# Performance work log

Measured on AMD Instinct MI355X. Metric: run time of the kernel, lower is better.

Reference implementation:

```python
import jax, jax.numpy as jnp
import numpy as np

N, L, S, E, A, D = 16, 256, 128, 128, 9, 768
ARG_ROLES = 23      # score width = ARG_ROLES + 1
MAX_ARG = 9         # hard-coded max_len_arg in the torch module
N_HID = 768


def setup_inputs() -> dict:
    key = jax.random.key(0)
    ks = jax.random.split(key, 10)
    all_embeddings = jax.random.normal(ks[0], (N, L, D), jnp.float32)
    # last-3-layer BERT attention maps, 12 heads, positive entries
    attn_last3 = jax.random.uniform(ks[1], (3, N, 12, L, L), jnp.float32)
    # per-sample sorted distinct first-subword indices (all positive, full length:
    # the ragged filter idxs>0 then keeps everything -> fixed-shape gather)
    idx_keys = jax.random.split(ks[2], N)
    cand = jnp.arange(1, L - MAX_ARG - 1)
    idxs_to_collect = jax.vmap(
        lambda k: jnp.sort(jax.random.choice(k, cand, (S + 2,), replace=False))
    )(idx_keys).astype(jnp.int32)
    is_triggers = (jax.random.uniform(ks[3], (N, S)) < 0.05).astype(jnp.float32)
    is_triggers = is_triggers.at[:, 0].set(1.0)  # >=1 trigger per sample
    entity_mapping = jax.random.normal(ks[4], (N, S, E), jnp.float32) * 0.05
    arg_weight_matrices = jax.random.normal(ks[5], (N, MAX_ARG, A), jnp.float32) * 0.3
    map_keys = jax.random.split(ks[6], N)
    arg_mapping = jax.vmap(
        lambda k: jax.random.permutation(k, ARG_ROLES + 1)[:A]
    )(map_keys).astype(jnp.int32)
    W1 = jax.random.normal(ks[7], (6 * D, N_HID), jnp.float32) * 0.02
    b1 = jnp.zeros((N_HID,), jnp.float32)
    W2 = jax.random.normal(ks[8], (N_HID, 1), jnp.float32) * 0.02
    b2 = jnp.zeros((1,), jnp.float32)
    return {
        "all_embeddings": all_embeddings,
        "attn_last3": attn_last3,
        "entity_mapping": entity_mapping,
        "arg_weight_matrices": arg_weight_matrices,
        "is_triggers": is_triggers,
        "W1": W1, "b1": b1, "W2": W2, "b2": b2,
        "idxs_to_collect": idxs_to_collect,
        "arg_mapping": arg_mapping,
    }


def reference(all_embeddings, attn_last3, entity_mapping, arg_weight_matrices,
              is_triggers, W1, b1, W2, b2, idxs_to_collect, arg_mapping):
    sqrt_d = jnp.sqrt(jnp.asarray(D, jnp.float32))
    sent_idx = idxs_to_collect[:, :S]                      # [N,S] first-subword ids
    # get_fist_subword_embeddings: ragged gather (full-length here)
    sent_emb = jnp.take_along_axis(all_embeddings, sent_idx[:, :, None], axis=1)  # [N,S,D]
    # arg-type tokens sit right after the second-to-last [SEP]
    arg_pos = idxs_to_collect[:, -2:-1] + 1 + jnp.arange(MAX_ARG)[None, :]        # [N,9]
    arg_raw = jnp.take_along_axis(all_embeddings, arg_pos[:, :, None], axis=1)    # [N,9,D]

    entity_emb = jnp.einsum('nsd,nse->ned', sent_emb, entity_mapping)             # [N,E,D]
    trig = jnp.sum(sent_emb * is_triggers[..., None], axis=1) \
           / jnp.sum(is_triggers, axis=1, keepdims=True)                          # [N,D]
    del trig  # _trigger is computed but unused downstream in the torch forward
    arg_emb = jnp.einsum('nkd,nka->nad', arg_raw, arg_weight_matrices)            # [N,A,D]

    # bi-attention scores (broadcast-mul-sum == contraction over D)
    t2a = jnp.einsum('ned,nad->nea', entity_emb, arg_emb) / sqrt_d
    w = (t2a - 5.0) / 2.0                                                         # [N,E,A]
    token_argAwared = jnp.einsum('nea,nad->ned', w, arg_emb)                      # [N,E,D]
    arg_tokenAwared = jnp.einsum('nea,ned->nad', w, entity_emb)                   # [N,A,D]

    # select_hidden_att for each of the last 3 layers
    att_mean = jnp.mean(attn_last3, axis=2)                                       # [3,N,L,L]
    def sel_layer(a):  # a: [N,L,L] -> row/col gather + row renorm
        s = jax.vmap(lambda m, i: m[i][:, i])(a, sent_idx)                        # [N,S,S]
        return s / (jnp.sum(s, axis=-1, keepdims=True) + 1e-9)
    t2t = (sel_layer(att_mean[0]) + sel_layer(att_mean[1]) + sel_layer(att_mean[2])) / 3.0

    h2h_sent = jnp.einsum('nst,ntd->nsd', t2t, sent_emb)                          # [N,S,D]
    # A_h2h and H_ are projected from sent space (S) to entity space (E)
    A_h2h_e = jnp.einsum('nsd,nse->ned', h2h_sent, entity_mapping)                # [N,E,D]
    H_e = entity_emb                                                              # sent_emb projected == entity_emb

    a2a = jax.nn.softmax(jnp.einsum('nad,nbd->nab', arg_emb, arg_emb), axis=-1)   # [N,A,A]
    u2u = jnp.einsum('nab,nbd->nad', a2a, arg_emb)                                # [N,A,D]

    shp = (N, E, A, D)
    H_    = jnp.broadcast_to(H_e[:, :, None, :], shp)
    U_    = jnp.broadcast_to(arg_emb[:, None, :, :], shp)
    A_h2u = jnp.broadcast_to(token_argAwared[:, :, None, :], shp)
    A_h2h = jnp.broadcast_to(A_h2h_e[:, :, None, :], shp)
    A_u2h = jnp.broadcast_to(arg_tokenAwared[:, None, :, :], shp)
    A_u2u = jnp.broadcast_to(u2u[:, None, :, :], shp)
    latent = jnp.concatenate([H_, U_, A_h2u, A_h2h, A_u2h, A_u2u], axis=-1)       # [N,E,A,6D]

    hid = jax.nn.gelu(latent @ W1 + b1, approximate=False)                        # [N,E,A,768]
    score = (hid @ W2 + b2)[..., 0]                                               # [N,E,A]

    # map_arg_to_ids: scatter each arg slot back to its global role id
    def scatter_one(s, ids):  # s [E,A], ids [A]
        return jnp.full((E, ARG_ROLES + 1), -1e6, jnp.float32).at[:, ids].set(s)
    new_score = jax.vmap(scatter_one)(score, arg_mapping)                         # [N,E,24]
    return new_score
```

## Files before the change

### kernel.cpp

```cpp
#include <hip/hip_runtime.h>
#include <math.h>

namespace {
constexpr int N_ = 16, L_ = 256, S_ = 128, E_ = 128, A_ = 9, D_ = 768, H_ = 768, RO_ = 24;
constexpr int IDXW = 130;
constexpr int W1R = 6 * D_;
constexpr float INV_SQRT_D = 0.03608439182435161f;
constexpr int PESZ = 2048 * 768;
constexpr int PASZ = 144 * 768;
constexpr int GB_T2T    = 0;
constexpr int GB_W1T    = 1024;
constexpr int GB_GATHER = 1888;
constexpr int GB_ENTMAP = 2080;
constexpr int GB_ARGU   = 2096;
constexpr int GB_TOTAL  = 2112;
}

using bshort8 = __attribute__((ext_vector_type(8))) short;
using f32x4v = __attribute__((ext_vector_type(4))) float;

__device__ __forceinline__ unsigned short f2bf(float f) {
    unsigned u = __builtin_bit_cast(unsigned, f);
    return (unsigned short)((u + 0x7fffu + ((u >> 16) & 1u)) >> 16);
}

__device__ __forceinline__ void gemm_body128(const unsigned short* __restrict__ A,
                                             const unsigned short* __restrict__ BT,
                                             int lda, int ldb, int c0, int tid,
                                             short (*As)[40], short (*Bs)[40],
                                             f32x4v acc[2][4]) {
    const int wave = tid >> 6, lane = tid & 63;
    const int row16 = lane & 15, quad = lane >> 4;
    for (int k0 = 0; k0 < S_; k0 += 32) {
#pragma unroll
        for (int i = 0; i < 2; ++i) {
            const int idx = tid + 256 * i;
            const int r = idx >> 2, q = idx & 3;
            *reinterpret_cast<bshort8*>(&As[r][q * 8]) =
                *reinterpret_cast<const bshort8*>(A + (size_t)r * lda + k0 + q * 8);
        }
        {
            const int col = tid >> 2, q = tid & 3;
            *reinterpret_cast<bshort8*>(&Bs[col][q * 8]) =
                *reinterpret_cast<const bshort8*>(BT + (size_t)(c0 + col) * ldb + k0 + q * 8);
        }
        __syncthreads();
        bshort8 a[2], b[4];
#pragma unroll
        for (int mi = 0; mi < 2; ++mi)
            a[mi] = *reinterpret_cast<const bshort8*>(&As[wave * 32 + mi * 16 + row16][quad * 8]);
#pragma unroll
        for (int ni = 0; ni < 4; ++ni)
            b[ni] = *reinterpret_cast<const bshort8*>(&Bs[ni * 16 + row16][quad * 8]);
#pragma unroll
        for (int mi = 0; mi < 2; ++mi)
#pragma unroll
            for (int ni = 0; ni < 4; ++ni)
                acc[mi][ni] = __builtin_amdgcn_mfma_f32_16x16x32_bf16(a[mi], b[ni], acc[mi][ni], 0, 0, 0);
        __syncthreads();
    }
}

__global__ __launch_bounds__(256) void stage1_k(const float* __restrict__ all_emb,
                                                const int* __restrict__ idxs,
                                                const float* __restrict__ ent_map,
                                                const float* __restrict__ W1,
                                                const float* __restrict__ argw,
                                                const float* __restrict__ attn,
                                                unsigned short* __restrict__ sentT,
                                                unsigned short* __restrict__ entmapT,
                                                short* __restrict__ W1t,
                                                unsigned short* __restrict__ t2tT,
                                                float* __restrict__ argE,
                                                unsigned short* __restrict__ argEbf,
                                                unsigned short* __restrict__ u2ubf) {
    __shared__ __align__(16) unsigned char smem[33792];
    const int b = blockIdx.x, tid = threadIdx.x;

    if (b < GB_W1T) {
        const int idx = b - GB_T2T;
        const int n = idx >> 6;
        const int half = tid >> 7, t128 = tid & 127;
        const int s0 = (idx & 63) << 1;
        const int s = s0 | half;
        const int w = t128 >> 6, lane = tid & 63;
        float* sum2 = (float*)smem;
        float* part = (float*)(smem + 12288);
        unsigned short* tileT = (unsigned short*)(smem + 12544);
        const int is = idxs[n * IDXW + s], it = idxs[n * IDXW + t128];
#pragma unroll
        for (int l = 0; l < 3; ++l) {
            const float* base = attn + ((size_t)((l * N_ + n) * 12 + w * 6)) * (L_ * L_)
                              + (size_t)is * L_ + lane * 4;
            float4 acc = {0.f, 0.f, 0.f, 0.f};
#pragma unroll
            for (int h = 0; h < 6; ++h) {
                const float4 v = *reinterpret_cast<const float4*>(base + (size_t)h * (L_ * L_));
                acc.x += v.x; acc.y += v.y; acc.z += v.z; acc.w += v.w;
            }
            *reinterpret_cast<float4*>(&sum2[(((half * 3 + l) * 2 + w) << 8) + lane * 4]) = acc;
        }
        __syncthreads();
        float m[3];
#pragma unroll
        for (int l = 0; l < 3; ++l) {
            m[l] = (sum2[(((half * 3 + l) * 2 + 0) << 8) + it] +
                    sum2[(((half * 3 + l) * 2 + 1) << 8) + it]) * (1.0f / 12.0f);
            float r = m[l];
#pragma unroll
            for (int off = 32; off; off >>= 1) r += __shfl_xor(r, off, 64);
            if (lane == 0) part[(half * 3 + l) * 2 + w] = r;
        }
        __syncthreads();
        float out = 0.f;
#pragma unroll
        for (int l = 0; l < 3; ++l)
            out += m[l] / (part[(half * 3 + l) * 2 + 0] + part[(half * 3 + l) * 2 + 1] + 1e-9f);
        tileT[t128 * 2 + half] = f2bf(out * (1.0f / 3.0f));
        __syncthreads();
        if (tid < 128) {
            const unsigned int v = ((const unsigned int*)tileT)[tid];
            *reinterpret_cast<unsigned int*>(t2tT + ((size_t)(n * S_) + tid) * S_ + s0) = v;
        }
    } else if (b < GB_GATHER) {
        const int b2 = b - GB_W1T;
        const int k0 = (b2 % 72) * 64, h0 = (b2 / 72) * 64;
        auto tile = (float (*)[65])smem;
        const int tx = tid & 63, ty = tid >> 6;
#pragma unroll
        for (int i = 0; i < 16; ++i) {
            const int r = ty + i * 4;
            tile[r][tx] = W1[(size_t)(k0 + r) * H_ + h0 + tx];
        }
        __syncthreads();
#pragma unroll
        for (int i = 0; i < 16; ++i) {
            const int r = ty + i * 4;
            W1t[(size_t)(h0 + r) * W1R + k0 + tx] = (short)f2bf(tile[tx][r]);
        }
    } else if (b < GB_ENTMAP) {
        const int b2 = b - GB_GATHER;
        const int n = b2 / 12, d0 = (b2 % 12) * 64;
        auto tile = (unsigned short (*)[132])smem;
#pragma unroll
        for (int it = 0; it < 8; ++it) {
            const int lin = tid + 256 * it;
            const int s = lin >> 4, dq = (lin & 15) * 4;
            const int row = idxs[n * IDXW + s];
            const float4 v = *reinterpret_cast<const float4*>(all_emb + ((size_t)(n * L_ + row)) * D_ + d0 + dq);
            tile[dq + 0][s] = f2bf(v.x); tile[dq + 1][s] = f2bf(v.y);
            tile[dq + 2][s] = f2bf(v.z); tile[dq + 3][s] = f2bf(v.w);
        }
        __syncthreads();
#pragma unroll
        for (int it = 0; it < 8; ++it) {
            const int lin = tid + 256 * it;
            const int d = lin >> 5, s4 = (lin & 31) * 4;
            ushort4 v = {tile[d][s4], tile[d][s4 + 1], tile[d][s4 + 2], tile[d][s4 + 3]};
            *reinterpret_cast<ushort4*>(sentT + ((size_t)(n * D_) + d0 + d) * S_ + s4) = v;
        }
    } else if (b < GB_ARGU) {
        const int n = b - GB_ENTMAP;
        auto tile = (unsigned short (*)[132])smem;
#pragma unroll
        for (int it = 0; it < 16; ++it) {
            const int lin = tid + 256 * it;
            const int s = lin >> 5, eq = (lin & 31) * 4;
            const float4 v = *reinterpret_cast<const float4*>(ent_map + ((size_t)(n * S_ + s)) * E_ + eq);
            tile[eq + 0][s] = f2bf(v.x); tile[eq + 1][s] = f2bf(v.y);
            tile[eq + 2][s] = f2bf(v.z); tile[eq + 3][s] = f2bf(v.w);
        }
        __syncthreads();
#pragma unroll
        for (int it = 0; it < 16; ++it) {
            const int lin = tid + 256 * it;
            const int e = lin >> 5, s4 = (lin & 31) * 4;
            ushort4 v = {tile[e][s4], tile[e][s4 + 1], tile[e][s4 + 2], tile[e][s4 + 3]};
            *reinterpret_cast<ushort4*>(entmapT + ((size_t)(n * E_) + e) * S_ + s4) = v;
        }
    } else {
        const int n = b - GB_ARGU;
        auto wsm = (float (*)[A_])smem;
        auto part45 = (float (*)[4])(smem + 512);
        auto Psm = (float (*)[A_])(smem + 1536);
        if (tid < A_ * A_) wsm[tid / A_][tid % A_] = argw[n * A_ * A_ + tid];
        __syncthreads();
        const int p0 = idxs[n * IDXW + S_] + 1;
        float pp[45] = {};
        float vals[3][A_];
#pragma unroll
        for (int c = 0; c < 3; ++c) {
            const int d = tid + 256 * c;
            float raw[A_];
#pragma unroll
            for (int k = 0; k < A_; ++k) raw[k] = all_emb[((size_t)(n * L_ + p0 + k)) * D_ + d];
#pragma unroll
            for (int a = 0; a < A_; ++a) {
                float acc = 0.f;
#pragma unroll
                for (int k = 0; k < A_; ++k) acc = fmaf(raw[k], wsm[k][a], acc);
                vals[c][a] = acc;
                argE[((size_t)(n * A_ + a)) * D_ + d] = acc;
                argEbf[((size_t)(n * A_ + a)) * D_ + d] = f2bf(acc);
            }
            int p = 0;
#pragma unroll
            for (int a = 0; a < A_; ++a)
#pragma unroll
                for (int bb = a; bb < A_; ++bb) pp[p++] += vals[c][a] * vals[c][bb];
        }
        const int lane = tid & 63, wv = tid >> 6;
#pragma unroll
        for (int p = 0; p < 45; ++p) {
            float v = pp[p];
            for (int off = 32; off; off >>= 1) v += __shfl_down(v, off, 64);
            if (lane == 0) part45[p][wv] = v;
        }
        __syncthreads();
        if (tid < 45) part45[tid][0] = part45[tid][0] + part45[tid][1] + part45[tid][2] + part45[tid][3];
        __syncthreads();
        if (tid < A_) {
            const int a = tid;
            float v[A_], mx = -1e30f;
#pragma unroll
            for (int bb = 0; bb < A_; ++bb) {
                const int lo = a < bb ? a : bb, hi = a < bb ? bb : a;
                v[bb] = part45[lo * (19 - lo) / 2 + hi - lo][0];
                mx = fmaxf(mx, v[bb]);
            }
            float sm = 0.f;
#pragma unroll
            for (int bb = 0; bb < A_; ++bb) { v[bb] = expf(v[bb] - mx); sm += v[bb]; }
            const float inv = 1.0f / sm;
#pragma unroll
            for (int bb = 0; bb < A_; ++bb) Psm[a][bb] = v[bb] * inv;
        }
        __syncthreads();
#pragma unroll
        for (int c = 0; c < 3; ++c) {
            const int d = tid + 256 * c;
#pragma unroll
            for (int a = 0; a < A_; ++a) {
                float acc = 0.f;
#pragma unroll
                for (int bb = 0; bb < A_; ++bb) acc = fmaf(Psm[a][bb], vals[c][bb], acc);
                u2ubf[((size_t)(n * A_ + a)) * D_ + d] = f2bf(acc);
            }
        }
    }
}

__global__ __launch_bounds__(256) void gemm_entM1_k(const unsigned short* __restrict__ entmapT,
                                                    const unsigned short* __restrict__ sentT,
                                                    const unsigned short* __restrict__ t2tT,
                                                    float* __restrict__ entf,
                                                    unsigned short* __restrict__ entbf,
                                                    unsigned short* __restrict__ M1bf) {
    __shared__ __align__(16) short As[128][40];
    __shared__ __align__(16) short Bs[64][40];
    const int bx = blockIdx.x, tid = threadIdx.x;
    const int wave = tid >> 6, lane = tid & 63;
    const int row16 = lane & 15, quad = lane >> 4;
    f32x4v acc[2][4] = {};
    if (bx < 192) {
        const int n = bx / 12, c0 = (bx % 12) * 64;
        gemm_body128(entmapT + (size_t)n * S_ * S_, sentT + (size_t)n * D_ * S_,
                     S_, S_, c0, tid, As, Bs, acc);
#pragma unroll
        for (int mi = 0; mi < 2; ++mi)
#pragma unroll
            for (int ni = 0; ni < 4; ++ni) {
                const int rbase = wave * 32 + mi * 16 + quad * 4;
                const int col = c0 + ni * 16 + row16;
#pragma unroll
                for (int t = 0; t < 4; ++t) {
                    const size_t o = ((size_t)(n * S_) + rbase + t) * D_ + col;
                    entf[o] = acc[mi][ni][t];
                    entbf[o] = f2bf(acc[mi][ni][t]);
                }
            }
    } else {
        const int idx = bx - 192;
        const int n = idx >> 1, c0 = (idx & 1) * 64;
        gemm_body128(entmapT + (size_t)n * S_ * S_, t2tT + (size_t)n * S_ * S_,
                     S_, S_, c0, tid, As, Bs, acc);
#pragma unroll
        for (int mi = 0; mi < 2; ++mi)
#pragma unroll
            for (int ni = 0; ni < 4; ++ni) {
                const int rbase = wave * 32 + mi * 16 + quad * 4;
                const int col = c0 + ni * 16 + row16;
#pragma unroll
                for (int t = 0; t < 4; ++t)
                    M1bf[((size_t)(n * S_) + rbase + t) * S_ + col] = f2bf(acc[mi][ni][t]);
            }
    }
}

__global__ __launch_bounds__(256) void fused3_k(const unsigned short* __restrict__ M1bf,
                                                const unsigned short* __restrict__ sentT,
                                                const float* __restrict__ entf,
                                                const float* __restrict__ argE,
                                                unsigned short* __restrict__ Ah2hbf,
                                                unsigned short* __restrict__ tokAbf,
                                                unsigned short* __restrict__ argTbf) {
    __shared__ __align__(16) unsigned char smem[15872];
    const int bx = blockIdx.x, tid = threadIdx.x;
    if (bx < N_ * A_) {
        const int n = bx / A_, a = bx % A_;
        float* argS = (float*)smem;
        float* wl = (float*)(smem + 3072);
        for (int i = tid; i < D_; i += 256) argS[i] = argE[((size_t)(n * A_ + a)) * D_ + i];
        __syncthreads();
        {
            const int e = tid >> 1, h = tid & 1;
            const float* er = entf + ((size_t)(n * E_ + e)) * D_ + h * 384;
            float p = 0.f;
            for (int d = 0; d < 384; ++d) p = fmaf(er[d], argS[h * 384 + d], p);
            p += __shfl_down(p, 1, 64);
            if (h == 0) wl[e] = (p * INV_SQRT_D - 5.0f) * 0.5f;
        }
        __syncthreads();
        const float* eb = entf + (size_t)n * E_ * D_;
#pragma unroll
        for (int c = 0; c < 3; ++c) {
            const int d = tid + 256 * c;
            float acc = 0.f;
            for (int e = 0; e < E_; ++e) acc = fmaf(wl[e], eb[(size_t)e * D_ + d], acc);
            argTbf[((size_t)(n * A_ + a)) * D_ + d] = f2bf(acc);
        }
    } else if (bx < N_ * A_ + 192) {
        const int idx = bx - N_ * A_;
        const int n = idx / 12, c0 = (idx % 12) * 64;
        short (*As)[40] = (short (*)[40])smem;
        short (*Bs)[40] = (short (*)[40])(smem + 10240);
        const int wave = tid >> 6, lane = tid & 63;
        const int row16 = lane & 15, quad = lane >> 4;
        f32x4v acc[2][4] = {};
        gemm_body128(M1bf + (size_t)n * S_ * S_, sentT + (size_t)n * D_ * S_,
                     S_, S_, c0, tid, As, Bs, acc);
#pragma unroll
        for (int mi = 0; mi < 2; ++mi)
#pragma unroll
            for (int ni = 0; ni < 4; ++ni) {
                const int rbase = wave * 32 + mi * 16 + quad * 4;
                const int col = c0 + ni * 16 + row16;
#pragma unroll
                for (int t = 0; t < 4; ++t)
                    Ah2hbf[((size_t)(n * S_) + rbase + t) * D_ + col] = f2bf(acc[mi][ni][t]);
            }
    } else {
        const int idx = bx - (N_ * A_ + 192);
        const int n = idx >> 7, e = idx & 127;
        float* wl = (float*)smem;
        float* part = (float*)(smem + 64);
        const float* er = entf + ((size_t)(n * E_ + e)) * D_;
        const float* ar = argE + (size_t)n * A_ * D_;
        float acc[A_] = {};
        for (int d = tid; d < D_; d += 256) {
            const float ev = er[d];
#pragma unroll
            for (int a = 0; a < A_; ++a) acc[a] = fmaf(ev, ar[(size_t)a * D_ + d], acc[a]);
        }
        const int lane = tid & 63, wv = tid >> 6;
#pragma unroll
        for (int a = 0; a < A_; ++a)
            for (int off = 32; off; off >>= 1) acc[a] += __shfl_down(acc[a], off, 64);
        if (lane == 0)
            for (int a = 0; a < A_; ++a) part[a * 4 + wv] = acc[a];
        __syncthreads();
        if (tid < A_)
            wl[tid] = ((part[tid * 4] + part[tid * 4 + 1] + part[tid * 4 + 2] + part[tid * 4 + 3])
                       * INV_SQRT_D - 5.0f) * 0.5f;
        __syncthreads();
#pragma unroll
        for (int c = 0; c < 3; ++c) {
            const int d = tid + 256 * c;
            float s = 0.f;
#pragma unroll
            for (int a = 0; a < A_; ++a) s = fmaf(wl[a], ar[(size_t)a * D_ + d], s);
            tokAbf[((size_t)(n * E_ + e)) * D_ + d] = f2bf(s);
        }
    }
}

__global__ __launch_bounds__(256) void mfma_mlp_k(const unsigned short* __restrict__ e0,
                                                  const unsigned short* __restrict__ e1,
                                                  const unsigned short* __restrict__ e2,
                                                  const unsigned short* __restrict__ a0,
                                                  const unsigned short* __restrict__ a1,
                                                  const unsigned short* __restrict__ a2,
                                                  const short* __restrict__ W1t,
                                                  float* __restrict__ Pe3, float* __restrict__ Pa3) {
    __shared__ __align__(16) short As[128][40];
    __shared__ __align__(16) short Bs[64][40];
    const int c0 = blockIdx.x * 64;
    const int by = blockIdx.y;
    const int seg = by / 18;
    const int blk = by % 18;
    const bool isPa = blk >= 16;
    const unsigned short* Aseg;
    int woff;
    if (isPa) {
        Aseg = seg == 0 ? a0 : (seg == 1 ? a1 : a2);
        woff = seg == 0 ? 1 * D_ : (seg == 1 ? 4 * D_ : 5 * D_);
    } else {
        Aseg = seg == 0 ? e0 : (seg == 1 ? e1 : e2);
        woff = seg == 0 ? 0 : (seg == 1 ? 2 * D_ : 3 * D_);
    }
    const int M = isPa ? N_ * A_ : N_ * E_;
    const int r0 = (isPa ? blk - 16 : blk) * 128;
    float* C = isPa ? (Pa3 + (size_t)seg * PASZ) : (Pe3 + (size_t)seg * PESZ);
    const int tid = threadIdx.x;
    const int wave = tid >> 6, lane = tid & 63;
    const int row16 = lane & 15, quad = lane >> 4;
    f32x4v acc[2][4] = {};
    for (int kk = 0; kk < D_; kk += 32) {
#pragma unroll
        for (int i = 0; i < 2; ++i) {
            const int idx = tid + 256 * i;
            const int r = idx >> 2, q = idx & 3;
            bshort8 av = {};
            if (r0 + r < M) av = *reinterpret_cast<const bshort8*>(Aseg + (size_t)(r0 + r) * D_ + kk + q * 8);
            *reinterpret_cast<bshort8*>(&As[r][q * 8]) = av;
        }
        {
            const int col = tid >> 2, q = tid & 3;
            *reinterpret_cast<bshort8*>(&Bs[col][q * 8]) =
                *reinterpret_cast<const bshort8*>(W1t + (size_t)(c0 + col) * W1R + woff + kk + q * 8);
        }
        __syncthreads();
        bshort8 a[2], b[4];
#pragma unroll
        for (int mi = 0; mi < 2; ++mi)
            a[mi] = *reinterpret_cast<const bshort8*>(&As[wave * 32 + mi * 16 + row16][quad * 8]);
#pragma unroll
        for (int ni = 0; ni < 4; ++ni)
            b[ni] = *reinterpret_cast<const bshort8*>(&Bs[ni * 16 + row16][quad * 8]);
#pragma unroll
        for (int mi = 0; mi < 2; ++mi)
#pragma unroll
            for (int ni = 0; ni < 4; ++ni)
                acc[mi][ni] = __builtin_amdgcn_mfma_f32_16x16x32_bf16(a[mi], b[ni], acc[mi][ni], 0, 0, 0);
        __syncthreads();
    }
#pragma unroll
    for (int mi = 0; mi < 2; ++mi) {
#pragma unroll
        for (int ni = 0; ni < 4; ++ni) {
            const int rbase = r0 + wave * 32 + mi * 16 + quad * 4;
            const int col = c0 + ni * 16 + row16;
#pragma unroll
            for (int t = 0; t < 4; ++t)
                if (rbase + t < M) C[(size_t)(rbase + t) * H_ + col] = acc[mi][ni][t];
        }
    }
}

__global__ __launch_bounds__(256) void score_k(const float* __restrict__ Pe3, const float* __restrict__ Pa3,
                                               const float* __restrict__ b1, const float* __restrict__ W2,
                                               const float* __restrict__ b2, const int* __restrict__ arg_map,
                                               float* __restrict__ out) {
    const int n = blockIdx.x >> 7, e = blockIdx.x & 127;
    const int tid = threadIdx.x;
    __shared__ float paS[A_ * H_];
    __shared__ float part[A_][4];
    float* orow = out + ((size_t)(n * E_ + e)) * RO_;
    if (tid < RO_) orow[tid] = -1000000.0f;
    for (int i = tid; i < A_ * H_; i += 256) {
        const size_t o = (size_t)n * A_ * H_ + i;
        paS[i] = Pa3[o] + Pa3[PASZ + o] + Pa3[2 * PASZ + o];
    }
    __syncthreads();
    const size_t ro = ((size_t)(n * E_ + e)) * H_;
    float acc[A_] = {};
    for (int h = tid; h < H_; h += 256) {
        const float pe = Pe3[ro + h] + Pe3[PESZ + ro + h] + Pe3[2 * PESZ + ro + h] + b1[h];
        const float w2 = W2[h];
#pragma unroll
        for (int a = 0; a < A_; ++a) {
            const float x = pe + paS[a * H_ + h];
            const float g = x * 0.5f * (1.0f + erff(x * 0.70710678118654752f));
            acc[a] = fmaf(g, w2, acc[a]);
        }
    }
    const int lane = tid & 63, wv = tid >> 6;
#pragma unroll
    for (int a = 0; a < A_; ++a)
        for (int off = 32; off; off >>= 1) acc[a] += __shfl_down(acc[a], off, 64);
    if (lane == 0)
        for (int a = 0; a < A_; ++a) part[a][wv] = acc[a];
    __syncthreads();
    if (tid < A_) {
        const float s = part[tid][0] + part[tid][1] + part[tid][2] + part[tid][3] + b2[0];
        orow[arg_map[n * A_ + tid]] = s;
    }
}

extern "C" void kernel_launch(void* const* d_in, const int* in_sizes, int n_in,
                              void* d_out, int out_size, void* d_ws, size_t ws_size,
                              hipStream_t stream) {
    const float* all_emb = (const float*)d_in[0];
    const float* attn    = (const float*)d_in[1];
    const float* ent_map = (const float*)d_in[2];
    const float* argw    = (const float*)d_in[3];
    const float* W1 = (const float*)d_in[5];
    const float* b1 = (const float*)d_in[6];
    const float* W2 = (const float*)d_in[7];
    const float* b2 = (const float*)d_in[8];
    const int* idxs    = (const int*)d_in[9];
    const int* arg_map = (const int*)d_in[10];
    float* out = (float*)d_out;

    float* ws = (float*)d_ws;
    float* entf = ws + 0;
    float* Pe3  = ws + 1572864;
    float* argE = ws + 6291456;
    float* Pa3  = ws + 6402048;
    short*          W1t     = (short*)(ws + 6733824);
    unsigned short* sentT   = (unsigned short*)(ws + 8503296);
    unsigned short* entmapT = (unsigned short*)(ws + 9289728);
    unsigned short* t2tT    = (unsigned short*)(ws + 9420800);
    unsigned short* M1bf    = (unsigned short*)(ws + 9551872);
    unsigned short* argEbf  = (unsigned short*)(ws + 9682944);
    unsigned short* u2ubf   = (unsigned short*)(ws + 9738240);
    unsigned short* entbf   = (unsigned short*)(ws + 9793536);
    unsigned short* Ah2hbf  = (unsigned short*)(ws + 10579968);
    unsigned short* tokAbf  = (unsigned short*)(ws + 11366400);
    unsigned short* argTbf  = (unsigned short*)(ws + 12152832);

    stage1_k<<<GB_TOTAL, 256, 0, stream>>>(all_emb, idxs, ent_map, W1, argw, attn,
                                           sentT, entmapT, W1t, t2tT, argE, argEbf, u2ubf);

    gemm_entM1_k<<<224, 256, 0, stream>>>(entmapT, sentT, t2tT, entf, entbf, M1bf);

    fused3_k<<<N_ * A_ + 192 + N_ * E_, 256, 0, stream>>>(M1bf, sentT, entf, argE,
                                                          Ah2hbf, tokAbf, argTbf);

    mfma_mlp_k<<<dim3(12, 54), 256, 0, stream>>>(entbf, tokAbf, Ah2hbf, argEbf, argTbf, u2ubf, W1t, Pe3, Pa3);

    score_k<<<N_ * E_, 256, 0, stream>>>(Pe3, Pa3, b1, W2, b2, arg_map, out);

    (void)in_sizes; (void)n_in; (void)out_size; (void)ws_size;
}
```

Before: 329.7 us.

## Fuse five stage kernels into one persistent kernel with grid barriers

```diff
diff --git a/kernel.cpp b/kernel.cpp
--- a/kernel.cpp
+++ b/kernel.cpp
@@ -24,6 +24,26 @@
     return (unsigned short)((u + 0x7fffu + ((u >> 16) & 1u)) >> 16);
 }
 
+__device__ __forceinline__ void gbar(unsigned* bar) {
+    __syncthreads();
+    if (threadIdx.x == 0) {
+        __threadfence();
+        const unsigned g = __hip_atomic_load(&bar[1], __ATOMIC_RELAXED, __HIP_MEMORY_SCOPE_AGENT);
+        const unsigned a = __hip_atomic_fetch_add(&bar[0], 1u, __ATOMIC_ACQ_REL, __HIP_MEMORY_SCOPE_AGENT);
+        if (a == gridDim.x - 1) {
+            __hip_atomic_store(&bar[0], 0u, __ATOMIC_RELAXED, __HIP_MEMORY_SCOPE_AGENT);
+            __hip_atomic_fetch_add(&bar[1], 1u, __ATOMIC_RELEASE, __HIP_MEMORY_SCOPE_AGENT);
+        } else {
+            unsigned spins = 0;
+            while (__hip_atomic_load(&bar[1], __ATOMIC_ACQUIRE, __HIP_MEMORY_SCOPE_AGENT) == g) {
+                if (++spins > 0x40000000u) break;
+            }
+        }
+        __threadfence();
+    }
+    __syncthreads();
+}
+
 __device__ __forceinline__ void gemm_body128(const unsigned short* __restrict__ A,
                                              const unsigned short* __restrict__ BT,
                                              int lda, int ldb, int c0, int tid,
@@ -61,306 +81,417 @@
     }
 }
 
-__global__ __launch_bounds__(256) void stage1_k(const float* __restrict__ all_emb,
-                                                const int* __restrict__ idxs,
-                                                const float* __restrict__ ent_map,
-                                                const float* __restrict__ W1,
-                                                const float* __restrict__ argw,
-                                                const float* __restrict__ attn,
-                                                unsigned short* __restrict__ sentT,
-                                                unsigned short* __restrict__ entmapT,
-                                                short* __restrict__ W1t,
-                                                unsigned short* __restrict__ t2tT,
-                                                float* __restrict__ argE,
-                                                unsigned short* __restrict__ argEbf,
-                                                unsigned short* __restrict__ u2ubf) {
+__global__ __launch_bounds__(256) void mega_k(
+    const float* __restrict__ all_emb, const float* __restrict__ attn,
+    const float* __restrict__ ent_map, const float* __restrict__ argw,
+    const float* __restrict__ W1, const float* __restrict__ b1,
+    const float* __restrict__ W2, const float* __restrict__ b2,
+    const int* __restrict__ idxs, const int* __restrict__ arg_map,
+    float* __restrict__ out,
+    float* __restrict__ entf, float* __restrict__ Pe3, float* __restrict__ argE,
+    float* __restrict__ Pa3, float* __restrict__ wbuf,
+    short* __restrict__ W1t,
+    unsigned short* __restrict__ sentT, unsigned short* __restrict__ entmapT,
+    unsigned short* __restrict__ t2tT, unsigned short* __restrict__ M1bf,
+    unsigned short* __restrict__ argEbf, unsigned short* __restrict__ u2ubf,
+    unsigned short* __restrict__ entbf, unsigned short* __restrict__ Ah2hbf,
+    unsigned short* __restrict__ tokAbf, unsigned short* __restrict__ argTbf,
+    unsigned* bar) {
     __shared__ __align__(16) unsigned char smem[33792];
-    const int b = blockIdx.x, tid = threadIdx.x;
-
-    if (b < GB_W1T) {
-        const int idx = b - GB_T2T;
-        const int n = idx >> 6;
-        const int half = tid >> 7, t128 = tid & 127;
-        const int s0 = (idx & 63) << 1;
-        const int s = s0 | half;
-        const int w = t128 >> 6, lane = tid & 63;
-        float* sum2 = (float*)smem;
-        float* part = (float*)(smem + 12288);
-        unsigned short* tileT = (unsigned short*)(smem + 12544);
-        const int is = idxs[n * IDXW + s], it = idxs[n * IDXW + t128];
-#pragma unroll
-        for (int l = 0; l < 3; ++l) {
-            const float* base = attn + ((size_t)((l * N_ + n) * 12 + w * 6)) * (L_ * L_)
-                              + (size_t)is * L_ + lane * 4;
-            float4 acc = {0.f, 0.f, 0.f, 0.f};
-#pragma unroll
-            for (int h = 0; h < 6; ++h) {
-                const float4 v = *reinterpret_cast<const float4*>(base + (size_t)h * (L_ * L_));
-                acc.x += v.x; acc.y += v.y; acc.z += v.z; acc.w += v.w;
-            }
-            *reinterpret_cast<float4*>(&sum2[(((half * 3 + l) * 2 + w) << 8) + lane * 4]) = acc;
-        }
-        __syncthreads();
-        float m[3];
-#pragma unroll
-        for (int l = 0; l < 3; ++l) {
-            m[l] = (sum2[(((half * 3 + l) * 2 + 0) << 8) + it] +
-                    sum2[(((half * 3 + l) * 2 + 1) << 8) + it]) * (1.0f / 12.0f);
-            float r = m[l];
-#pragma unroll
-            for (int off = 32; off; off >>= 1) r += __shfl_xor(r, off, 64);
-            if (lane == 0) part[(half * 3 + l) * 2 + w] = r;
-        }
-        __syncthreads();
-        float out = 0.f;
-#pragma unroll
-        for (int l = 0; l < 3; ++l)
-            out += m[l] / (part[(half * 3 + l) * 2 + 0] + part[(half * 3 + l) * 2 + 1] + 1e-9f);
-        tileT[t128 * 2 + half] = f2bf(out * (1.0f / 3.0f));
-        __syncthreads();
-        if (tid < 128) {
-            const unsigned int v = ((const unsigned int*)tileT)[tid];
-            *reinterpret_cast<unsigned int*>(t2tT + ((size_t)(n * S_) + tid) * S_ + s0) = v;
-        }
-    } else if (b < GB_GATHER) {
-        const int b2 = b - GB_W1T;
-        const int k0 = (b2 % 72) * 64, h0 = (b2 / 72) * 64;
-        auto tile = (float (*)[65])smem;
-        const int tx = tid & 63, ty = tid >> 6;
-#pragma unroll
-        for (int i = 0; i < 16; ++i) {
-            const int r = ty + i * 4;
-            tile[r][tx] = W1[(size_t)(k0 + r) * H_ + h0 + tx];
-        }
-        __syncthreads();
-#pragma unroll
-        for (int i = 0; i < 16; ++i) {
-            const int r = ty + i * 4;
-            W1t[(size_t)(h0 + r) * W1R + k0 + tx] = (short)f2bf(tile[tx][r]);
-        }
-    } else if (b < GB_ENTMAP) {
-        const int b2 = b - GB_GATHER;
-        const int n = b2 / 12, d0 = (b2 % 12) * 64;
-        auto tile = (unsigned short (*)[132])smem;
-#pragma unroll
-        for (int it = 0; it < 8; ++it) {
-            const int lin = tid + 256 * it;
-            const int s = lin >> 4, dq = (lin & 15) * 4;
-            const int row = idxs[n * IDXW + s];
-            const float4 v = *reinterpret_cast<const float4*>(all_emb + ((size_t)(n * L_ + row)) * D_ + d0 + dq);
-            tile[dq + 0][s] = f2bf(v.x); tile[dq + 1][s] = f2bf(v.y);
-            tile[dq + 2][s] = f2bf(v.z); tile[dq + 3][s] = f2bf(v.w);
-        }
-        __syncthreads();
-#pragma unroll
-        for (int it = 0; it < 8; ++it) {
-            const int lin = tid + 256 * it;
-            const int d = lin >> 5, s4 = (lin & 31) * 4;
-            ushort4 v = {tile[d][s4], tile[d][s4 + 1], tile[d][s4 + 2], tile[d][s4 + 3]};
-            *reinterpret_cast<ushort4*>(sentT + ((size_t)(n * D_) + d0 + d) * S_ + s4) = v;
-        }
-    } else if (b < GB_ARGU) {
-        const int n = b - GB_ENTMAP;
-        auto tile = (unsigned short (*)[132])smem;
-#pragma unroll
-        for (int it = 0; it < 16; ++it) {
-            const int lin = tid + 256 * it;
-            const int s = lin >> 5, eq = (lin & 31) * 4;
-            const float4 v = *reinterpret_cast<const float4*>(ent_map + ((size_t)(n * S_ + s)) * E_ + eq);
-            tile[eq + 0][s] = f2bf(v.x); tile[eq + 1][s] = f2bf(v.y);
-            tile[eq + 2][s] = f2bf(v.z); tile[eq + 3][s] = f2bf(v.w);
-        }
-        __syncthreads();
-#pragma unroll
-        for (int it = 0; it < 16; ++it) {
-            const int lin = tid + 256 * it;
-            const int e = lin >> 5, s4 = (lin & 31) * 4;
-            ushort4 v = {tile[e][s4], tile[e][s4 + 1], tile[e][s4 + 2], tile[e][s4 + 3]};
-            *reinterpret_cast<ushort4*>(entmapT + ((size_t)(n * E_) + e) * S_ + s4) = v;
-        }
-    } else {
-        const int n = b - GB_ARGU;
-        auto wsm = (float (*)[A_])smem;
-        auto part45 = (float (*)[4])(smem + 512);
-        auto Psm = (float (*)[A_])(smem + 1536);
-        if (tid < A_ * A_) wsm[tid / A_][tid % A_] = argw[n * A_ * A_ + tid];
-        __syncthreads();
-        const int p0 = idxs[n * IDXW + S_] + 1;
-        float pp[45] = {};
-        float vals[3][A_];
-#pragma unroll
-        for (int c = 0; c < 3; ++c) {
-            const int d = tid + 256 * c;
-            float raw[A_];
-#pragma unroll
-            for (int k = 0; k < A_; ++k) raw[k] = all_emb[((size_t)(n * L_ + p0 + k)) * D_ + d];
-#pragma unroll
-            for (int a = 0; a < A_; ++a) {
-                float acc = 0.f;
-#pragma unroll
-                for (int k = 0; k < A_; ++k) acc = fmaf(raw[k], wsm[k][a], acc);
-                vals[c][a] = acc;
-                argE[((size_t)(n * A_ + a)) * D_ + d] = acc;
-                argEbf[((size_t)(n * A_ + a)) * D_ + d] = f2bf(acc);
-            }
-            int p = 0;
-#pragma unroll
-            for (int a = 0; a < A_; ++a)
-#pragma unroll
-                for (int bb = a; bb < A_; ++bb) pp[p++] += vals[c][a] * vals[c][bb];
-        }
-        const int lane = tid & 63, wv = tid >> 6;
-#pragma unroll
-        for (int p = 0; p < 45; ++p) {
-            float v = pp[p];
-            for (int off = 32; off; off >>= 1) v += __shfl_down(v, off, 64);
-            if (lane == 0) part45[p][wv] = v;
-        }
-        __syncthreads();
-        if (tid < 45) part45[tid][0] = part45[tid][0] + part45[tid][1] + part45[tid][2] + part45[tid][3];
-        __syncthreads();
-        if (tid < A_) {
-            const int a = tid;
-            float v[A_], mx = -1e30f;
-#pragma unroll
-            for (int bb = 0; bb < A_; ++bb) {
-                const int lo = a < bb ? a : bb, hi = a < bb ? bb : a;
-                v[bb] = part45[lo * (19 - lo) / 2 + hi - lo][0];
-                mx = fmaxf(mx, v[bb]);
-            }
-            float sm = 0.f;
-#pragma unroll
-            for (int bb = 0; bb < A_; ++bb) { v[bb] = expf(v[bb] - mx); sm += v[bb]; }
-            const float inv = 1.0f / sm;
-#pragma unroll
-            for (int bb = 0; bb < A_; ++bb) Psm[a][bb] = v[bb] * inv;
-        }
-        __syncthreads();
-#pragma unroll
-        for (int c = 0; c < 3; ++c) {
-            const int d = tid + 256 * c;
-#pragma unroll
-            for (int a = 0; a < A_; ++a) {
-                float acc = 0.f;
-#pragma unroll
-                for (int bb = 0; bb < A_; ++bb) acc = fmaf(Psm[a][bb], vals[c][bb], acc);
-                u2ubf[((size_t)(n * A_ + a)) * D_ + d] = f2bf(acc);
-            }
-        }
-    }
-}
-
-__global__ __launch_bounds__(256) void gemm_entM1_k(const unsigned short* __restrict__ entmapT,
-                                                    const unsigned short* __restrict__ sentT,
-                                                    const unsigned short* __restrict__ t2tT,
-                                                    float* __restrict__ entf,
-                                                    unsigned short* __restrict__ entbf,
-                                                    unsigned short* __restrict__ M1bf) {
-    __shared__ __align__(16) short As[128][40];
-    __shared__ __align__(16) short Bs[64][40];
-    const int bx = blockIdx.x, tid = threadIdx.x;
-    const int wave = tid >> 6, lane = tid & 63;
-    const int row16 = lane & 15, quad = lane >> 4;
-    f32x4v acc[2][4] = {};
-    if (bx < 192) {
-        const int n = bx / 12, c0 = (bx % 12) * 64;
-        gemm_body128(entmapT + (size_t)n * S_ * S_, sentT + (size_t)n * D_ * S_,
-                     S_, S_, c0, tid, As, Bs, acc);
-#pragma unroll
-        for (int mi = 0; mi < 2; ++mi)
-#pragma unroll
-            for (int ni = 0; ni < 4; ++ni) {
-                const int rbase = wave * 32 + mi * 16 + quad * 4;
-                const int col = c0 + ni * 16 + row16;
-#pragma unroll
-                for (int t = 0; t < 4; ++t) {
-                    const size_t o = ((size_t)(n * S_) + rbase + t) * D_ + col;
-                    entf[o] = acc[mi][ni][t];
-                    entbf[o] = f2bf(acc[mi][ni][t]);
-                }
-            }
-    } else {
-        const int idx = bx - 192;
-        const int n = idx >> 1, c0 = (idx & 1) * 64;
-        gemm_body128(entmapT + (size_t)n * S_ * S_, t2tT + (size_t)n * S_ * S_,
-                     S_, S_, c0, tid, As, Bs, acc);
-#pragma unroll
-        for (int mi = 0; mi < 2; ++mi)
-#pragma unroll
-            for (int ni = 0; ni < 4; ++ni) {
-                const int rbase = wave * 32 + mi * 16 + quad * 4;
-                const int col = c0 + ni * 16 + row16;
-#pragma unroll
-                for (int t = 0; t < 4; ++t)
-                    M1bf[((size_t)(n * S_) + rbase + t) * S_ + col] = f2bf(acc[mi][ni][t]);
-            }
-    }
-}
-
-__global__ __launch_bounds__(256) void fused3_k(const unsigned short* __restrict__ M1bf,
-                                                const unsigned short* __restrict__ sentT,
-                                                const float* __restrict__ entf,
-                                                const float* __restrict__ argE,
-                                                unsigned short* __restrict__ Ah2hbf,
-                                                unsigned short* __restrict__ tokAbf,
-                                                unsigned short* __restrict__ argTbf) {
-    __shared__ __align__(16) unsigned char smem[15872];
-    const int bx = blockIdx.x, tid = threadIdx.x;
-    if (bx < N_ * A_) {
-        const int n = bx / A_, a = bx % A_;
-        float* argS = (float*)smem;
-        float* wl = (float*)(smem + 3072);
-        for (int i = tid; i < D_; i += 256) argS[i] = argE[((size_t)(n * A_ + a)) * D_ + i];
-        __syncthreads();
-        {
-            const int e = tid >> 1, h = tid & 1;
-            const float* er = entf + ((size_t)(n * E_ + e)) * D_ + h * 384;
-            float p = 0.f;
-            for (int d = 0; d < 384; ++d) p = fmaf(er[d], argS[h * 384 + d], p);
-            p += __shfl_down(p, 1, 64);
-            if (h == 0) wl[e] = (p * INV_SQRT_D - 5.0f) * 0.5f;
-        }
-        __syncthreads();
-        const float* eb = entf + (size_t)n * E_ * D_;
-#pragma unroll
-        for (int c = 0; c < 3; ++c) {
-            const int d = tid + 256 * c;
-            float acc = 0.f;
-            for (int e = 0; e < E_; ++e) acc = fmaf(wl[e], eb[(size_t)e * D_ + d], acc);
-            argTbf[((size_t)(n * A_ + a)) * D_ + d] = f2bf(acc);
-        }
-    } else if (bx < N_ * A_ + 192) {
-        const int idx = bx - N_ * A_;
-        const int n = idx / 12, c0 = (idx % 12) * 64;
+    const int G = gridDim.x, tid = threadIdx.x;
+
+    for (int b = blockIdx.x; b < GB_TOTAL; b += G) {
+        if (b < GB_W1T) {
+            const int idx = b - GB_T2T;
+            const int n = idx >> 6;
+            const int half = tid >> 7, t128 = tid & 127;
+            const int s0 = (idx & 63) << 1;
+            const int s = s0 | half;
+            const int w = t128 >> 6, lane = tid & 63;
+            float* sum2 = (float*)smem;
+            float* part = (float*)(smem + 12288);
+            unsigned short* tileT = (unsigned short*)(smem + 12544);
+            const int is = idxs[n * IDXW + s], it = idxs[n * IDXW + t128];
+#pragma unroll
+            for (int l = 0; l < 3; ++l) {
+                const float* base = attn + ((size_t)((l * N_ + n) * 12 + w * 6)) * (L_ * L_)
+                                  + (size_t)is * L_ + lane * 4;
+                float4 acc = {0.f, 0.f, 0.f, 0.f};
+#pragma unroll
+                for (int h = 0; h < 6; ++h) {
+                    const float4 v = *reinterpret_cast<const float4*>(base + (size_t)h * (L_ * L_));
+                    acc.x += v.x; acc.y += v.y; acc.z += v.z; acc.w += v.w;
+                }
+                *reinterpret_cast<float4*>(&sum2[(((half * 3 + l) * 2 + w) << 8) + lane * 4]) = acc;
+            }
+            __syncthreads();
+            float m[3];
+#pragma unroll
+            for (int l = 0; l < 3; ++l) {
+                m[l] = (sum2[(((half * 3 + l) * 2 + 0) << 8) + it] +
+                        sum2[(((half * 3 + l) * 2 + 1) << 8) + it]) * (1.0f / 12.0f);
+                float r = m[l];
+#pragma unroll
+                for (int off = 32; off; off >>= 1) r += __shfl_xor(r, off, 64);
+                if (lane == 0) part[(half * 3 + l) * 2 + w] = r;
+            }
+            __syncthreads();
+            float o = 0.f;
+#pragma unroll
+            for (int l = 0; l < 3; ++l)
+                o += m[l] / (part[(half * 3 + l) * 2 + 0] + part[(half * 3 + l) * 2 + 1] + 1e-9f);
+            tileT[t128 * 2 + half] = f2bf(o * (1.0f / 3.0f));
+            __syncthreads();
+            if (tid < 128) {
+                const unsigned int v = ((const unsigned int*)tileT)[tid];
+                *reinterpret_cast<unsigned int*>(t2tT + ((size_t)(n * S_) + tid) * S_ + s0) = v;
+            }
+        } else if (b < GB_GATHER) {
+            const int b2 = b - GB_W1T;
+            const int k0 = (b2 % 72) * 64, h0 = (b2 / 72) * 64;
+            auto tile = (float (*)[65])smem;
+            const int tx = tid & 63, ty = tid >> 6;
+#pragma unroll
+            for (int i = 0; i < 16; ++i) {
+                const int r = ty + i * 4;
+                tile[r][tx] = W1[(size_t)(k0 + r) * H_ + h0 + tx];
+            }
+            __syncthreads();
+#pragma unroll
+            for (int i = 0; i < 16; ++i) {
+                const int r = ty + i * 4;
+                W1t[(size_t)(h0 + r) * W1R + k0 + tx] = (short)f2bf(tile[tx][r]);
+            }
+        } else if (b < GB_ENTMAP) {
+            const int b2 = b - GB_GATHER;
+            const int n = b2 / 12, d0 = (b2 % 12) * 64;
+            auto tile = (unsigned short (*)[132])smem;
+#pragma unroll
+            for (int it = 0; it < 8; ++it) {
+                const int lin = tid + 256 * it;
+                const int s = lin >> 4, dq = (lin & 15) * 4;
+                const int row = idxs[n * IDXW + s];
+                const float4 v = *reinterpret_cast<const float4*>(all_emb + ((size_t)(n * L_ + row)) * D_ + d0 + dq);
+                tile[dq + 0][s] = f2bf(v.x); tile[dq + 1][s] = f2bf(v.y);
+                tile[dq + 2][s] = f2bf(v.z); tile[dq + 3][s] = f2bf(v.w);
+            }
+            __syncthreads();
+#pragma unroll
+            for (int it = 0; it < 8; ++it) {
+                const int lin = tid + 256 * it;
+                const int d = lin >> 5, s4 = (lin & 31) * 4;
+                ushort4 v = {tile[d][s4], tile[d][s4 + 1], tile[d][s4 + 2], tile[d][s4 + 3]};
+                *reinterpret_cast<ushort4*>(sentT + ((size_t)(n * D_) + d0 + d) * S_ + s4) = v;
+            }
+        } else if (b < GB_ARGU) {
+            const int n = b - GB_ENTMAP;
+            auto tile = (unsigned short (*)[132])smem;
+#pragma unroll
+            for (int it = 0; it < 16; ++it) {
+                const int lin = tid + 256 * it;
+                const int s = lin >> 5, eq = (lin & 31) * 4;
+                const float4 v = *reinterpret_cast<const float4*>(ent_map + ((size_t)(n * S_ + s)) * E_ + eq);
+                tile[eq + 0][s] = f2bf(v.x); tile[eq + 1][s] = f2bf(v.y);
+                tile[eq + 2][s] = f2bf(v.z); tile[eq + 3][s] = f2bf(v.w);
+            }
+            __syncthreads();
+#pragma unroll
+            for (int it = 0; it < 16; ++it) {
+                const int lin = tid + 256 * it;
+                const int e = lin >> 5, s4 = (lin & 31) * 4;
+                ushort4 v = {tile[e][s4], tile[e][s4 + 1], tile[e][s4 + 2], tile[e][s4 + 3]};
+                *reinterpret_cast<ushort4*>(entmapT + ((size_t)(n * E_) + e) * S_ + s4) = v;
+            }
+        } else {
+            const int n = b - GB_ARGU;
+            auto wsm = (float (*)[A_])smem;
+            auto part45 = (float (*)[4])(smem + 512);
+            auto Psm = (float (*)[A_])(smem + 1536);
+            if (tid < A_ * A_) wsm[tid / A_][tid % A_] = argw[n * A_ * A_ + tid];
+            __syncthreads();
+            const int p0 = idxs[n * IDXW + S_] + 1;
+            float pp[45] = {};
+            float vals[3][A_];
+#pragma unroll
+            for (int c = 0; c < 3; ++c) {
+                const int d = tid + 256 * c;
+                float raw[A_];
+#pragma unroll
+                for (int k = 0; k < A_; ++k) raw[k] = all_emb[((size_t)(n * L_ + p0 + k)) * D_ + d];
+#pragma unroll
+                for (int a = 0; a < A_; ++a) {
+                    float acc = 0.f;
+#pragma unroll
+                    for (int k = 0; k < A_; ++k) acc = fmaf(raw[k], wsm[k][a], acc);
+                    vals[c][a] = acc;
+                    argE[((size_t)(n * A_ + a)) * D_ + d] = acc;
+                    argEbf[((size_t)(n * A_ + a)) * D_ + d] = f2bf(acc);
+                }
+                int p = 0;
+#pragma unroll
+                for (int a = 0; a < A_; ++a)
+#pragma unroll
+                    for (int bb = a; bb < A_; ++bb) pp[p++] += vals[c][a] * vals[c][bb];
+            }
+            const int lane = tid & 63, wv = tid >> 6;
+#pragma unroll
+            for (int p = 0; p < 45; ++p) {
+                float v = pp[p];
+                for (int off = 32; off; off >>= 1) v += __shfl_down(v, off, 64);
+                if (lane == 0) part45[p][wv] = v;
+            }
+            __syncthreads();
+            if (tid < 45) part45[tid][0] = part45[tid][0] + part45[tid][1] + part45[tid][2] + part45[tid][3];
+            __syncthreads();
+            if (tid < A_) {
+                const int a = tid;
+                float v[A_], mx = -1e30f;
+#pragma unroll
+                for (int bb = 0; bb < A_; ++bb) {
+                    const int lo = a < bb ? a : bb, hi = a < bb ? bb : a;
+                    v[bb] = part45[lo * (19 - lo) / 2 + hi - lo][0];
+                    mx = fmaxf(mx, v[bb]);
+                }
+                float sm = 0.f;
+#pragma unroll
+                for (int bb = 0; bb < A_; ++bb) { v[bb] = expf(v[bb] - mx); sm += v[bb]; }
+                const float inv = 1.0f / sm;
+#pragma unroll
+                for (int bb = 0; bb < A_; ++bb) Psm[a][bb] = v[bb] * inv;
+            }
+            __syncthreads();
+#pragma unroll
+            for (int c = 0; c < 3; ++c) {
+                const int d = tid + 256 * c;
+#pragma unroll
+                for (int a = 0; a < A_; ++a) {
+                    float acc = 0.f;
+#pragma unroll
+                    for (int bb = 0; bb < A_; ++bb) acc = fmaf(Psm[a][bb], vals[c][bb], acc);
+                    u2ubf[((size_t)(n * A_ + a)) * D_ + d] = f2bf(acc);
+                }
+            }
+        }
+        __syncthreads();
+    }
+    gbar(bar);
+
+    for (int b = blockIdx.x; b < 224; b += G) {
         short (*As)[40] = (short (*)[40])smem;
         short (*Bs)[40] = (short (*)[40])(smem + 10240);
         const int wave = tid >> 6, lane = tid & 63;
         const int row16 = lane & 15, quad = lane >> 4;
         f32x4v acc[2][4] = {};
-        gemm_body128(M1bf + (size_t)n * S_ * S_, sentT + (size_t)n * D_ * S_,
-                     S_, S_, c0, tid, As, Bs, acc);
-#pragma unroll
-        for (int mi = 0; mi < 2; ++mi)
+        if (b < 192) {
+            const int n = b / 12, c0 = (b % 12) * 64;
+            gemm_body128(entmapT + (size_t)n * S_ * S_, sentT + (size_t)n * D_ * S_,
+                         S_, S_, c0, tid, As, Bs, acc);
+#pragma unroll
+            for (int mi = 0; mi < 2; ++mi)
+#pragma unroll
+                for (int ni = 0; ni < 4; ++ni) {
+                    const int rbase = wave * 32 + mi * 16 + quad * 4;
+                    const int col = c0 + ni * 16 + row16;
+#pragma unroll
+                    for (int t = 0; t < 4; ++t) {
+                        const size_t o = ((size_t)(n * S_) + rbase + t) * D_ + col;
+                        entf[o] = acc[mi][ni][t];
+                        entbf[o] = f2bf(acc[mi][ni][t]);
+                    }
+                }
+        } else {
+            const int idx = b - 192;
+            const int n = idx >> 1, c0 = (idx & 1) * 64;
+            gemm_body128(entmapT + (size_t)n * S_ * S_, t2tT + (size_t)n * S_ * S_,
+                         S_, S_, c0, tid, As, Bs, acc);
+#pragma unroll
+            for (int mi = 0; mi < 2; ++mi)
+#pragma unroll
+                for (int ni = 0; ni < 4; ++ni) {
+                    const int rbase = wave * 32 + mi * 16 + quad * 4;
+                    const int col = c0 + ni * 16 + row16;
+#pragma unroll
+                    for (int t = 0; t < 4; ++t)
+                        M1bf[((size_t)(n * S_) + rbase + t) * S_ + col] = f2bf(acc[mi][ni][t]);
+                }
+        }
+        __syncthreads();
+    }
+    gbar(bar);
+
+    for (int b = blockIdx.x; b < 208; b += G) {
+        const int wave = tid >> 6, lane = tid & 63;
+        const int row16 = lane & 15, quad = lane >> 4;
+        if (b < 192) {
+            short (*As)[40] = (short (*)[40])smem;
+            short (*Bs)[40] = (short (*)[40])(smem + 10240);
+            const int n = b / 12, c0 = (b % 12) * 64;
+            f32x4v acc[2][4] = {};
+            gemm_body128(M1bf + (size_t)n * S_ * S_, sentT + (size_t)n * D_ * S_,
+                         S_, S_, c0, tid, As, Bs, acc);
+#pragma unroll
+            for (int mi = 0; mi < 2; ++mi)
+#pragma unroll
+                for (int ni = 0; ni < 4; ++ni) {
+                    const int rbase = wave * 32 + mi * 16 + quad * 4;
+                    const int col = c0 + ni * 16 + row16;
+#pragma unroll
+                    for (int t = 0; t < 4; ++t)
+                        Ah2hbf[((size_t)(n * S_) + rbase + t) * D_ + col] = f2bf(acc[mi][ni][t]);
+                }
+        } else {
+            const int n = b - 192;
+            const unsigned short* Aent = entbf + (size_t)n * E_ * D_;
+            const unsigned short* Barg = argEbf + (size_t)n * A_ * D_;
+            f32x4v acc[2] = {};
+            for (int k0 = 0; k0 < D_; k0 += 32) {
+                bshort8 a[2], bb;
+#pragma unroll
+                for (int mi = 0; mi < 2; ++mi)
+                    a[mi] = *reinterpret_cast<const bshort8*>(Aent + (size_t)(wave * 32 + mi * 16 + row16) * D_ + k0 + quad * 8);
+                bb = *reinterpret_cast<const bshort8*>(Barg + (size_t)row16 * D_ + k0 + quad * 8);
+#pragma unroll
+                for (int mi = 0; mi < 2; ++mi)
+                    acc[mi] = __builtin_amdgcn_mfma_f32_16x16x32_bf16(a[mi], bb, acc[mi], 0, 0, 0);
+            }
+            if (row16 < A_) {
+#pragma unroll
+                for (int mi = 0; mi < 2; ++mi)
+#pragma unroll
+                    for (int t = 0; t < 4; ++t) {
+                        const int e = wave * 32 + mi * 16 + quad * 4 + t;
+                        const float w = (acc[mi][t] * INV_SQRT_D - 5.0f) * 0.5f;
+                        wbuf[((size_t)(n * E_ + e)) * A_ + row16] = w;
+                    }
+            }
+        }
+        __syncthreads();
+    }
+    gbar(bar);
+
+    for (int b = blockIdx.x; b < N_ * E_ + N_ * A_; b += G) {
+        if (b < N_ * E_) {
+            const int n = b >> 7, e = b & 127;
+            float* wl = (float*)smem;
+            if (tid < A_) wl[tid] = wbuf[(size_t)(n * E_ + e) * A_ + tid];
+            __syncthreads();
+            const float* ar = argE + (size_t)n * A_ * D_;
+#pragma unroll
+            for (int c = 0; c < 3; ++c) {
+                const int d = tid + 256 * c;
+                float s = 0.f;
+#pragma unroll
+                for (int a = 0; a < A_; ++a) s = fmaf(wl[a], ar[(size_t)a * D_ + d], s);
+                tokAbf[((size_t)(n * E_ + e)) * D_ + d] = f2bf(s);
+            }
+        } else {
+            const int idx = b - N_ * E_;
+            const int n = idx / A_, a = idx % A_;
+            float* wl = (float*)smem;
+            if (tid < E_) wl[tid] = wbuf[(size_t)(n * E_ + tid) * A_ + a];
+            __syncthreads();
+            const float* eb = entf + (size_t)n * E_ * D_;
+#pragma unroll
+            for (int c = 0; c < 3; ++c) {
+                const int d = tid + 256 * c;
+                float acc = 0.f;
+                for (int e = 0; e < E_; ++e) acc = fmaf(wl[e], eb[(size_t)e * D_ + d], acc);
+                argTbf[((size_t)(n * A_ + a)) * D_ + d] = f2bf(acc);
+            }
+        }
+        __syncthreads();
+    }
+    gbar(bar);
+
+    for (int b = blockIdx.x; b < 648; b += G) {
+        short (*As)[40] = (short (*)[40])smem;
+        short (*Bs)[40] = (short (*)[40])(smem + 10240);
+        const int segblk = b % 54;
+        const int c0 = (b / 54) * 64;
+        const int seg = segblk % 3;
+        const int blk = segblk / 3;
+        const bool isPa = blk >= 16;
+        const unsigned short* Aseg;
+        int woff;
+        if (isPa) {
+            Aseg = seg == 0 ? argEbf : (seg == 1 ? argTbf : u2ubf);
+            woff = seg == 0 ? 1 * D_ : (seg == 1 ? 4 * D_ : 5 * D_);
+        } else {
+            Aseg = seg == 0 ? entbf : (seg == 1 ? tokAbf : Ah2hbf);
+            woff = seg == 0 ? 0 : (seg == 1 ? 2 * D_ : 3 * D_);
+        }
+        const int M = isPa ? N_ * A_ : N_ * E_;
+        const int r0 = (isPa ? blk - 16 : blk) * 128;
+        float* C = isPa ? (Pa3 + (size_t)seg * PASZ) : (Pe3 + (size_t)seg * PESZ);
+        const int wave = tid >> 6, lane = tid & 63;
+        const int row16 = lane & 15, quad = lane >> 4;
+        f32x4v acc[2][4] = {};
+        for (int kk = 0; kk < D_; kk += 32) {
+#pragma unroll
+            for (int i = 0; i < 2; ++i) {
+                const int idx = tid + 256 * i;
+                const int r = idx >> 2, q = idx & 3;
+                bshort8 av = {};
+                if (r0 + r < M) av = *reinterpret_cast<const bshort8*>(Aseg + (size_t)(r0 + r) * D_ + kk + q * 8);
+                *reinterpret_cast<bshort8*>(&As[r][q * 8]) = av;
+            }
+            {
+                const int col = tid >> 2, q = tid & 3;
+                *reinterpret_cast<bshort8*>(&Bs[col][q * 8]) =
+                    *reinterpret_cast<const bshort8*>(W1t + (size_t)(c0 + col) * W1R + woff + kk + q * 8);
+            }
+            __syncthreads();
+            bshort8 a[2], bb[4];
+#pragma unroll
+            for (int mi = 0; mi < 2; ++mi)
+                a[mi] = *reinterpret_cast<const bshort8*>(&As[wave * 32 + mi * 16 + row16][quad * 8]);
+#pragma unroll
+            for (int ni = 0; ni < 4; ++ni)
+                bb[ni] = *reinterpret_cast<const bshort8*>(&Bs[ni * 16 + row16][quad * 8]);
+#pragma unroll
+            for (int mi = 0; mi < 2; ++mi)
+#pragma unroll
+                for (int ni = 0; ni < 4; ++ni)
+                    acc[mi][ni] = __builtin_amdgcn_mfma_f32_16x16x32_bf16(a[mi], bb[ni], acc[mi][ni], 0, 0, 0);
+            __syncthreads();
+        }
+#pragma unroll
+        for (int mi = 0; mi < 2; ++mi) {
 #pragma unroll
             for (int ni = 0; ni < 4; ++ni) {
-                const int rbase = wave * 32 + mi * 16 + quad * 4;
+                const int rbase = r0 + wave * 32 + mi * 16 + quad * 4;
                 const int col = c0 + ni * 16 + row16;
 #pragma unroll
                 for (int t = 0; t < 4; ++t)
-                    Ah2hbf[((size_t)(n * S_) + rbase + t) * D_ + col] = f2bf(acc[mi][ni][t]);
-            }
-    } else {
-        const int idx = bx - (N_ * A_ + 192);
-        const int n = idx >> 7, e = idx & 127;
-        float* wl = (float*)smem;
-        float* part = (float*)(smem + 64);
-        const float* er = entf + ((size_t)(n * E_ + e)) * D_;
-        const float* ar = argE + (size_t)n * A_ * D_;
+                    if (rbase + t < M) C[(size_t)(rbase + t) * H_ + col] = acc[mi][ni][t];
+            }
+        }
+        __syncthreads();
+    }
+    gbar(bar);
+
+    for (int b = blockIdx.x; b < N_ * E_; b += G) {
+        const int n = b >> 7, e = b & 127;
+        float* paS = (float*)smem;
+        float* part = (float*)(smem + 27648);
+        float* orow = out + ((size_t)(n * E_ + e)) * RO_;
+        if (tid < RO_) orow[tid] = -1000000.0f;
+        for (int i = tid; i < A_ * H_; i += 256) {
+            const size_t o = (size_t)n * A_ * H_ + i;
+            paS[i] = Pa3[o] + Pa3[PASZ + o] + Pa3[2 * PASZ + o];
+        }
+        __syncthreads();
+        const size_t ro = ((size_t)(n * E_ + e)) * H_;
         float acc[A_] = {};
-        for (int d = tid; d < D_; d += 256) {
-            const float ev = er[d];
-#pragma unroll
-            for (int a = 0; a < A_; ++a) acc[a] = fmaf(ev, ar[(size_t)a * D_ + d], acc[a]);
+        for (int h = tid; h < H_; h += 256) {
+            const float pe = Pe3[ro + h] + Pe3[PESZ + ro + h] + Pe3[2 * PESZ + ro + h] + b1[h];
+            const float w2 = W2[h];
+#pragma unroll
+            for (int a = 0; a < A_; ++a) {
+                const float x = pe + paS[a * H_ + h];
+                const float g = x * 0.5f * (1.0f + erff(x * 0.70710678118654752f));
+                acc[a] = fmaf(g, w2, acc[a]);
+            }
         }
         const int lane = tid & 63, wv = tid >> 6;
 #pragma unroll
@@ -369,131 +500,11 @@
         if (lane == 0)
             for (int a = 0; a < A_; ++a) part[a * 4 + wv] = acc[a];
         __syncthreads();
-        if (tid < A_)
-            wl[tid] = ((part[tid * 4] + part[tid * 4 + 1] + part[tid * 4 + 2] + part[tid * 4 + 3])
-                       * INV_SQRT_D - 5.0f) * 0.5f;
-        __syncthreads();
-#pragma unroll
-        for (int c = 0; c < 3; ++c) {
-            const int d = tid + 256 * c;
-            float s = 0.f;
-#pragma unroll
-            for (int a = 0; a < A_; ++a) s = fmaf(wl[a], ar[(size_t)a * D_ + d], s);
-            tokAbf[((size_t)(n * E_ + e)) * D_ + d] = f2bf(s);
-        }
-    }
-}
-
-__global__ __launch_bounds__(256) void mfma_mlp_k(const unsigned short* __restrict__ e0,
-                                                  const unsigned short* __restrict__ e1,
-                                                  const unsigned short* __restrict__ e2,
-                                                  const unsigned short* __restrict__ a0,
-                                                  const unsigned short* __restrict__ a1,
-                                                  const unsigned short* __restrict__ a2,
-                                                  const short* __restrict__ W1t,
-                                                  float* __restrict__ Pe3, float* __restrict__ Pa3) {
-    __shared__ __align__(16) short As[128][40];
-    __shared__ __align__(16) short Bs[64][40];
-    const int c0 = blockIdx.x * 64;
-    const int by = blockIdx.y;
-    const int seg = by / 18;
-    const int blk = by % 18;
-    const bool isPa = blk >= 16;
-    const unsigned short* Aseg;
-    int woff;
-    if (isPa) {
-        Aseg = seg == 0 ? a0 : (seg == 1 ? a1 : a2);
-        woff = seg == 0 ? 1 * D_ : (seg == 1 ? 4 * D_ : 5 * D_);
-    } else {
-        Aseg = seg == 0 ? e0 : (seg == 1 ? e1 : e2);
-        woff = seg == 0 ? 0 : (seg == 1 ? 2 * D_ : 3 * D_);
-    }
-    const int M = isPa ? N_ * A_ : N_ * E_;
-    const int r0 = (isPa ? blk - 16 : blk) * 128;
-    float* C = isPa ? (Pa3 + (size_t)seg * PASZ) : (Pe3 + (size_t)seg * PESZ);
-    const int tid = threadIdx.x;
-    const int wave = tid >> 6, lane = tid & 63;
-    const int row16 = lane & 15, quad = lane >> 4;
-    f32x4v acc[2][4] = {};
-    for (int kk = 0; kk < D_; kk += 32) {
-#pragma unroll
-        for (int i = 0; i < 2; ++i) {
-            const int idx = tid + 256 * i;
-            const int r = idx >> 2, q = idx & 3;
-            bshort8 av = {};
-            if (r0 + r < M) av = *reinterpret_cast<const bshort8*>(Aseg + (size_t)(r0 + r) * D_ + kk + q * 8);
-            *reinterpret_cast<bshort8*>(&As[r][q * 8]) = av;
-        }
-        {
-            const int col = tid >> 2, q = tid & 3;
-            *reinterpret_cast<bshort8*>(&Bs[col][q * 8]) =
-                *reinterpret_cast<const bshort8*>(W1t + (size_t)(c0 + col) * W1R + woff + kk + q * 8);
-        }
-        __syncthreads();
-        bshort8 a[2], b[4];
-#pragma unroll
-        for (int mi = 0; mi < 2; ++mi)
-            a[mi] = *reinterpret_cast<const bshort8*>(&As[wave * 32 + mi * 16 + row16][quad * 8]);
-#pragma unroll
-        for (int ni = 0; ni < 4; ++ni)
-            b[ni] = *reinterpret_cast<const bshort8*>(&Bs[ni * 16 + row16][quad * 8]);
-#pragma unroll
-        for (int mi = 0; mi < 2; ++mi)
-#pragma unroll
-            for (int ni = 0; ni < 4; ++ni)
-                acc[mi][ni] = __builtin_amdgcn_mfma_f32_16x16x32_bf16(a[mi], b[ni], acc[mi][ni], 0, 0, 0);
-        __syncthreads();
-    }
-#pragma unroll
-    for (int mi = 0; mi < 2; ++mi) {
-#pragma unroll
-        for (int ni = 0; ni < 4; ++ni) {
-            const int rbase = r0 + wave * 32 + mi * 16 + quad * 4;
-            const int col = c0 + ni * 16 + row16;
-#pragma unroll
-            for (int t = 0; t < 4; ++t)
-                if (rbase + t < M) C[(size_t)(rbase + t) * H_ + col] = acc[mi][ni][t];
-        }
-    }
-}
-
-__global__ __launch_bounds__(256) void score_k(const float* __restrict__ Pe3, const float* __restrict__ Pa3,
-                                               const float* __restrict__ b1, const float* __restrict__ W2,
-                                               const float* __restrict__ b2, const int* __restrict__ arg_map,
-                                               float* __restrict__ out) {
-    const int n = blockIdx.x >> 7, e = blockIdx.x & 127;
-    const int tid = threadIdx.x;
-    __shared__ float paS[A_ * H_];
-    __shared__ float part[A_][4];
-    float* orow = out + ((size_t)(n * E_ + e)) * RO_;
-    if (tid < RO_) orow[tid] = -1000000.0f;
-    for (int i = tid; i < A_ * H_; i += 256) {
-        const size_t o = (size_t)n * A_ * H_ + i;
-        paS[i] = Pa3[o] + Pa3[PASZ + o] + Pa3[2 * PASZ + o];
-    }
-    __syncthreads();
-    const size_t ro = ((size_t)(n * E_ + e)) * H_;
-    float acc[A_] = {};
-    for (int h = tid; h < H_; h += 256) {
-        const float pe = Pe3[ro + h] + Pe3[PESZ + ro + h] + Pe3[2 * PESZ + ro + h] + b1[h];
-        const float w2 = W2[h];
-#pragma unroll
-        for (int a = 0; a < A_; ++a) {
-            const float x = pe + paS[a * H_ + h];
-            const float g = x * 0.5f * (1.0f + erff(x * 0.70710678118654752f));
-            acc[a] = fmaf(g, w2, acc[a]);
-        }
-    }
-    const int lane = tid & 63, wv = tid >> 6;
-#pragma unroll
-    for (int a = 0; a < A_; ++a)
-        for (int off = 32; off; off >>= 1) acc[a] += __shfl_down(acc[a], off, 64);
-    if (lane == 0)
-        for (int a = 0; a < A_; ++a) part[a][wv] = acc[a];
-    __syncthreads();
-    if (tid < A_) {
-        const float s = part[tid][0] + part[tid][1] + part[tid][2] + part[tid][3] + b2[0];
-        orow[arg_map[n * A_ + tid]] = s;
+        if (tid < A_) {
+            const float s = part[tid * 4] + part[tid * 4 + 1] + part[tid * 4 + 2] + part[tid * 4 + 3] + b2[0];
+            orow[arg_map[n * A_ + tid]] = s;
+        }
+        __syncthreads();
     }
 }
 
@@ -517,29 +528,35 @@
     float* Pe3  = ws + 1572864;
     float* argE = ws + 6291456;
     float* Pa3  = ws + 6402048;
-    short*          W1t     = (short*)(ws + 6733824);
-    unsigned short* sentT   = (unsigned short*)(ws + 8503296);
-    unsigned short* entmapT = (unsigned short*)(ws + 9289728);
-    unsigned short* t2tT    = (unsigned short*)(ws + 9420800);
-    unsigned short* M1bf    = (unsigned short*)(ws + 9551872);
-    unsigned short* argEbf  = (unsigned short*)(ws + 9682944);
-    unsigned short* u2ubf   = (unsigned short*)(ws + 9738240);
-    unsigned short* entbf   = (unsigned short*)(ws + 9793536);
-    unsigned short* Ah2hbf  = (unsigned short*)(ws + 10579968);
-    unsigned short* tokAbf  = (unsigned short*)(ws + 11366400);
-    unsigned short* argTbf  = (unsigned short*)(ws + 12152832);
-
-    stage1_k<<<GB_TOTAL, 256, 0, stream>>>(all_emb, idxs, ent_map, W1, argw, attn,
-                                           sentT, entmapT, W1t, t2tT, argE, argEbf, u2ubf);
-
-    gemm_entM1_k<<<224, 256, 0, stream>>>(entmapT, sentT, t2tT, entf, entbf, M1bf);
-
-    fused3_k<<<N_ * A_ + 192 + N_ * E_, 256, 0, stream>>>(M1bf, sentT, entf, argE,
-                                                          Ah2hbf, tokAbf, argTbf);
-
-    mfma_mlp_k<<<dim3(12, 54), 256, 0, stream>>>(entbf, tokAbf, Ah2hbf, argEbf, argTbf, u2ubf, W1t, Pe3, Pa3);
-
-    score_k<<<N_ * E_, 256, 0, stream>>>(Pe3, Pa3, b1, W2, b2, arg_map, out);
+    float* wbuf = ws + 6733824;
+    short*          W1t     = (short*)(ws + 6752256);
+    unsigned short* sentT   = (unsigned short*)(ws + 8521728);
+    unsigned short* entmapT = (unsigned short*)(ws + 9308160);
+    unsigned short* t2tT    = (unsigned short*)(ws + 9439232);
+    unsigned short* M1bf    = (unsigned short*)(ws + 9570304);
+    unsigned short* argEbf  = (unsigned short*)(ws + 9701376);
+    unsigned short* u2ubf   = (unsigned short*)(ws + 9756672);
+    unsigned short* entbf   = (unsigned short*)(ws + 9811968);
+    unsigned short* Ah2hbf  = (unsigned short*)(ws + 10598400);
+    unsigned short* tokAbf  = (unsigned short*)(ws + 11384832);
+    unsigned short* argTbf  = (unsigned short*)(ws + 12171264);
+    unsigned*       bar     = (unsigned*)(ws + 12226560);
+
+    static int bpc = 0;
+    if (bpc == 0) {
+        int nb = 0;
+        if (hipOccupancyMaxActiveBlocksPerMultiprocessor(&nb, mega_k, 256, 0) != hipSuccess || nb < 1) nb = 1;
+        if (nb > 4) nb = 4;
+        bpc = nb;
+    }
+    const int G = bpc * 256;
+
+    hipMemsetAsync((void*)bar, 0, 64, stream);
+    mega_k<<<G, 256, 0, stream>>>(all_emb, attn, ent_map, argw, W1, b1, W2, b2,
+                                  idxs, arg_map, out,
+                                  entf, Pe3, argE, Pa3, wbuf, W1t,
+                                  sentT, entmapT, t2tT, M1bf, argEbf, u2ubf,
+                                  entbf, Ah2hbf, tokAbf, argTbf, bar);
 
     (void)in_sizes; (void)n_in; (void)out_size; (void)ws_size;
 }
```

After: 666.8 us. +102.3%, slower.
